# Kernel tuning notes

Measured on AMD Instinct MI355X. Metric: run time of the kernel, lower is better.

## Reference

```python
import jax, jax.numpy as jnp
import numpy as np

B = 4096
SEQ = 128            # window_size * rnn_in_pkts
WINDOW = 32
IN_PKTS = 4
LEN_V, LEN_E = 1500, 64
IPD_V, IPD_E = 256, 64
EV = 64              # embedding_vector_bits
RNN_IN = IN_PKTS * EV   # 256
H = 256              # rnn_hidden_bits
LABELS = 100


def setup_inputs() -> dict:
    key = jax.random.key(0)
    ks = jax.random.split(key, 12)
    s = 0.05
    return {
        "len_x": jax.random.randint(ks[0], (B, SEQ), 0, LEN_V),
        "ipd_x": jax.random.randint(ks[1], (B, SEQ), 0, IPD_V),
        "len_emb": jax.random.normal(ks[2], (LEN_V, LEN_E), jnp.float32) * s,
        "ipd_emb": jax.random.normal(ks[3], (IPD_V, IPD_E), jnp.float32) * s,
        "fc_w": jax.random.normal(ks[4], (EV, LEN_E + IPD_E), jnp.float32) * s,
        "fc_b": jax.random.normal(ks[5], (EV,), jnp.float32) * s,
        "w_ih": jax.random.normal(ks[6], (3 * H, RNN_IN), jnp.float32) * s,
        "w_hh": jax.random.normal(ks[7], (3 * H, H), jnp.float32) * s,
        "b_ih": jax.random.normal(ks[8], (3 * H,), jnp.float32) * s,
        "b_hh": jax.random.normal(ks[9], (3 * H,), jnp.float32) * s,
        "out_w": jax.random.normal(ks[10], (LABELS, H), jnp.float32) * s,
        "out_b": jax.random.normal(ks[11], (LABELS,), jnp.float32) * s,
    }


def _gru_scan(rnn_in, w_ih, w_hh, b_ih, b_hh):
    # rnn_in: [B, T, RNN_IN]. Precompute input-side gates for all steps at once.
    gi_all = jnp.einsum("bti,gi->btg", rnn_in, w_ih) + b_ih  # [B,T,3H]
    h0 = jnp.zeros((rnn_in.shape[0], H), rnn_in.dtype)

    def step(h, gi):
        gh = h @ w_hh.T + b_hh                 # [B,3H]
        i_r, i_z, i_n = jnp.split(gi, 3, axis=-1)
        h_r, h_z, h_n = jnp.split(gh, 3, axis=-1)
        r = jax.nn.sigmoid(i_r + h_r)
        z = jax.nn.sigmoid(i_z + h_z)
        n = jnp.tanh(i_n + r * h_n)
        h_new = (1.0 - z) * n + z * h
        return h_new, None

    h_final, _ = jax.lax.scan(step, h0, jnp.swapaxes(gi_all, 0, 1))
    return h_final


def reference(len_x, ipd_x, len_emb, ipd_emb, fc_w, fc_b, w_ih, w_hh, b_ih, b_hh, out_w, out_b):
    len_e = len_emb[len_x]                      # [B,SEQ,LEN_E]
    ipd_e = ipd_emb[ipd_x]                      # [B,SEQ,IPD_E]
    cat = jnp.concatenate([len_e, ipd_e], axis=-1)
    evs = cat @ fc_w.T + fc_b                   # [B,SEQ,EV]
    rnn_in = evs.reshape(B, WINDOW, RNN_IN)     # [B,32,256]
    h = _gru_scan(rnn_in, w_ih, w_hh, b_ih, b_hh)
    logits = h @ out_w.T + out_b                # [B,LABELS]
    return logits
```

## Files before the change

kernel.cpp:

```cpp
#include <hip/hip_runtime.h>
#include <hip/hip_bf16.h>

typedef __bf16 bf16_t;
typedef __bf16 bf16x8 __attribute__((ext_vector_type(8)));
typedef float f32x4 __attribute__((ext_vector_type(4)));
typedef unsigned short u16x4 __attribute__((ext_vector_type(4)));

#define MFMA16(a, b, c) __builtin_amdgcn_mfma_f32_16x16x32_bf16((a), (b), (c), 0, 0, 0)

#define BATCH 4096
#define SEQN 128
#define HN 256
#define NLABELS 100
#define TSTEPS 32
#define LEN_VN 1500
#define IPD_VN 256

#define OFF_LENT   0u
#define OFF_IPDT   384000u
#define OFF_BRZ    449536u
#define OFF_WIH    451584u
#define OFF_WHH    844800u
#define OFF_GI     1238016u
#define WS_NEEDED  202564608u

__device__ __forceinline__ float sigf(float x) {
    return __builtin_amdgcn_rcpf(1.f + __expf(-x));
}
__device__ __forceinline__ float tanh_fast(float x) {
    return 2.f * __builtin_amdgcn_rcpf(1.f + __expf(-2.f * x)) - 1.f;
}
__device__ __forceinline__ float b2f(unsigned short v) {
    union { unsigned u; float f; } c; c.u = ((unsigned)v) << 16; return c.f;
}
__device__ __forceinline__ unsigned short f2b(float f) {
    union { bf16_t h; unsigned short s; } c; c.h = (bf16_t)f; return c.s;
}

__global__ void prep_kernel(const float* __restrict__ len_emb,
                            const float* __restrict__ ipd_emb,
                            const float* __restrict__ fc_w,
                            const float* __restrict__ fc_b,
                            const float* __restrict__ w_ih,
                            const float* __restrict__ w_hh,
                            const float* __restrict__ b_ih,
                            const float* __restrict__ b_hh,
                            float* __restrict__ lenT, float* __restrict__ ipdT,
                            float* __restrict__ brz,
                            bf16_t* __restrict__ wfrag_ih,
                            bf16_t* __restrict__ wfrag_hh) {
    const int bid = blockIdx.x, tid = threadIdx.x;
    if (bid < 439) {
        const int row = bid * 4 + (tid >> 6);
        const int e = tid & 63;
        if (row < LEN_VN) {
            const float* emb = len_emb + row * 64;
            const float* wv = fc_w + e * 128;
            float s = fc_b[e];
            #pragma unroll 8
            for (int j = 0; j < 64; ++j) s += emb[j] * wv[j];
            lenT[row * 64 + e] = s;
        } else if (row < LEN_VN + IPD_VN) {
            const int v = row - LEN_VN;
            const float* emb = ipd_emb + v * 64;
            const float* wv = fc_w + e * 128 + 64;
            float s = 0.f;
            #pragma unroll 8
            for (int j = 0; j < 64; ++j) s += emb[j] * wv[j];
            ipdT[v * 64 + e] = s;
        }
    } else if (bid < 631) {
        const int flat = (bid - 439) * 256 + tid;
        const int which = flat / 24576;
        const int rem = flat % 24576;
        const int c = rem >> 9;
        const int kt = (rem >> 6) & 7;
        const int lane = rem & 63;
        const int g = c * 16 + (lane & 15);
        const int k0 = kt * 32 + (lane >> 4) * 8;
        const float* src = (which == 0 ? w_ih : w_hh) + g * 256 + k0;
        bf16_t* dst = (which == 0 ? wfrag_ih : wfrag_hh) + ((c * 8 + kt) * 64 + lane) * 8;
        f32x4 s0 = *(const f32x4*)(src);
        f32x4 s1 = *(const f32x4*)(src + 4);
        bf16x8 o;
        #pragma unroll
        for (int j = 0; j < 4; ++j) { o[j] = (bf16_t)s0[j]; o[4 + j] = (bf16_t)s1[j]; }
        *(bf16x8*)dst = o;
    } else {
        const int g = (bid - 631) * 256 + tid;
        if (g < 512) brz[g] = b_ih[g] + b_hh[g];
    }
}

__global__ void __launch_bounds__(512, 2)
gemm_gi(const int* __restrict__ len_x, const int* __restrict__ ipd_x,
        const float* __restrict__ lenT, const float* __restrict__ ipdT,
        const bf16_t* __restrict__ wfrag_ih, bf16_t* __restrict__ gi) {
    __shared__ bf16_t wlds[8 * 8 * 512];
    __shared__ bf16_t a_lds[2][8 * 512];

    const int tid = threadIdx.x;
    const int lane = tid & 63;
    const int w = tid >> 6;
    const int bt = blockIdx.x;

    const int cts[6] = {2*w, 2*w + 1, 16 + 2*w, 17 + 2*w, 32 + 2*w, 33 + 2*w};

    bf16x8 wr[5][8];
    #pragma unroll
    for (int cc = 0; cc < 5; ++cc)
        #pragma unroll
        for (int kt = 0; kt < 8; ++kt)
            wr[cc][kt] = *(const bf16x8*)(wfrag_ih + ((cts[cc] * 8 + kt) * 64 + lane) * 8);
    #pragma unroll
    for (int kt = 0; kt < 8; ++kt)
        *(bf16x8*)&wlds[(w * 8 + kt) * 512 + lane * 8] =
            *(const bf16x8*)(wfrag_ih + ((cts[5] * 8 + kt) * 64 + lane) * 8);

    const int b_row = bt * 16 + (lane & 15);
    const int k0 = w * 32 + (lane >> 4) * 8;
    const int p = k0 >> 6;
    const int e0 = k0 & 63;
    auto do_gather = [&](int t, int buf) {
        const int seq = t * 4 + p;
        const int v1 = len_x[b_row * SEQN + seq];
        const int v2 = ipd_x[b_row * SEQN + seq];
        const f32x4* lp = (const f32x4*)(lenT + v1 * 64 + e0);
        const f32x4* ip = (const f32x4*)(ipdT + v2 * 64 + e0);
        f32x4 a0 = lp[0] + ip[0];
        f32x4 a1 = lp[1] + ip[1];
        bf16x8 o;
        #pragma unroll
        for (int j = 0; j < 4; ++j) { o[j] = (bf16_t)a0[j]; o[4 + j] = (bf16_t)a1[j]; }
        *(bf16x8*)&a_lds[buf][tid * 8] = o;
    };

    do_gather(0, 0);
    bf16_t* gib = gi + (size_t)bt * 32 * 48 * 256 + lane * 4;

    for (int t = 0; t < TSTEPS; ++t) {
        const int cur = t & 1;
        __syncthreads();
        if (t + 1 < TSTEPS) do_gather(t + 1, cur ^ 1);

        f32x4 acc[6] = {};
        #pragma unroll
        for (int kt = 0; kt < 8; ++kt) {
            bf16x8 af = *(const bf16x8*)&a_lds[cur][kt * 512 + lane * 8];
            bf16x8 w5 = *(const bf16x8*)&wlds[(w * 8 + kt) * 512 + lane * 8];
            #pragma unroll
            for (int cc = 0; cc < 5; ++cc)
                acc[cc] = MFMA16(af, wr[cc][kt], acc[cc]);
            acc[5] = MFMA16(af, w5, acc[5]);
        }

        #pragma unroll
        for (int cc = 0; cc < 6; ++cc) {
            u16x4 o;
            #pragma unroll
            for (int r = 0; r < 4; ++r) o[r] = f2b(acc[cc][r]);
            *(u16x4*)(gib + ((size_t)t * 48 + cts[cc]) * 256) = o;
        }
    }
}

__global__ void __launch_bounds__(512, 2)
gru_kernel(const bf16_t* __restrict__ gi,
           const bf16_t* __restrict__ wfrag_hh,
           const float* __restrict__ brz,
           const float* __restrict__ b_ih,
           const float* __restrict__ b_hh,
           const float* __restrict__ out_w,
           const float* __restrict__ out_b,
           float* __restrict__ out) {
    __shared__ bf16_t wlds[8 * 8 * 512];
    __shared__ bf16_t h_lds[8 * 512];
    __shared__ float h_fin[16 * 260];

    const int tid = threadIdx.x;
    const int lane = tid & 63;
    const int w = tid >> 6;
    const int bt = blockIdx.x;
    const int col = lane & 15;
    const int jbase = w * 32;

    const int cts[6] = {2*w, 2*w + 1, 16 + 2*w, 17 + 2*w, 32 + 2*w, 33 + 2*w};

    bf16x8 wr[5][8];
    #pragma unroll
    for (int cc = 0; cc < 5; ++cc)
        #pragma unroll
        for (int kt = 0; kt < 8; ++kt)
            wr[cc][kt] = *(const bf16x8*)(wfrag_hh + ((cts[cc] * 8 + kt) * 64 + lane) * 8);
    #pragma unroll
    for (int kt = 0; kt < 8; ++kt)
        *(bf16x8*)&wlds[(w * 8 + kt) * 512 + lane * 8] =
            *(const bf16x8*)(wfrag_hh + ((cts[5] * 8 + kt) * 64 + lane) * 8);

    for (int i = tid; i < 8 * 512; i += 512) h_lds[i] = (bf16_t)0.f;

    float b_r[2], b_z[2], b_in[2], b_hn[2];
    #pragma unroll
    for (int c2 = 0; c2 < 2; ++c2) {
        const int j = jbase + c2 * 16 + col;
        b_r[c2] = brz[j];
        b_z[c2] = brz[256 + j];
        b_in[c2] = b_ih[512 + j];
        b_hn[c2] = b_hh[512 + j];
    }

    f32x4 hprev[2] = {};
    const bf16_t* gib = gi + (size_t)bt * 32 * 48 * 256 + lane * 4;

    for (int t = 0; t < TSTEPS; ++t) {
        u16x4 g[6];
        #pragma unroll
        for (int cc = 0; cc < 6; ++cc)
            g[cc] = *(const u16x4*)(gib + ((size_t)t * 48 + cts[cc]) * 256);

        f32x4 acc[6] = {};
        __syncthreads();
        #pragma unroll
        for (int kt = 0; kt < 8; ++kt) {
            bf16x8 ah = *(const bf16x8*)&h_lds[kt * 512 + lane * 8];
            bf16x8 w5 = *(const bf16x8*)&wlds[(w * 8 + kt) * 512 + lane * 8];
            #pragma unroll
            for (int cc = 0; cc < 5; ++cc)
                acc[cc] = MFMA16(ah, wr[cc][kt], acc[cc]);
            acc[5] = MFMA16(ah, w5, acc[5]);
        }
        __syncthreads();

        #pragma unroll
        for (int c2 = 0; c2 < 2; ++c2) {
            const int j = jbase + c2 * 16 + col;
            const int kt_j = j >> 5;
            const int lane_j = ((j >> 3) & 3) * 16;
            const int jj = j & 7;
            #pragma unroll
            for (int r = 0; r < 4; ++r) {
                float rg = sigf(acc[c2][r] + b2f(g[c2][r]) + b_r[c2]);
                float zg = sigf(acc[2 + c2][r] + b2f(g[2 + c2][r]) + b_z[c2]);
                float u = b2f(g[4 + c2][r]) + b_in[c2] + rg * (acc[4 + c2][r] + b_hn[c2]);
                float ng = tanh_fast(u);
                float hn = (1.f - zg) * ng + zg * hprev[c2][r];
                hprev[c2][r] = hn;
                const int m = ((lane >> 4) << 2) + r;
                h_lds[kt_j * 512 + (lane_j + m) * 8 + jj] = (bf16_t)hn;
            }
        }
    }

    #pragma unroll
    for (int c2 = 0; c2 < 2; ++c2) {
        const int j = jbase + c2 * 16 + col;
        #pragma unroll
        for (int r = 0; r < 4; ++r) {
            const int m = ((lane >> 4) << 2) + r;
            h_fin[m * 260 + j] = hprev[c2][r];
        }
    }
    __syncthreads();

    for (int i = tid; i < 16 * NLABELS; i += 512) {
        const int row = i / NLABELS;
        const int cl = i - row * NLABELS;
        const f32x4* wrow = (const f32x4*)(out_w + cl * 256);
        const f32x4* hr = (const f32x4*)(h_fin + row * 260);
        f32x4 acc = {0.f, 0.f, 0.f, 0.f};
        #pragma unroll 4
        for (int k = 0; k < 64; ++k) acc += hr[k] * wrow[k];
        out[(bt * 16 + row) * NLABELS + cl] =
            out_b[cl] + acc[0] + acc[1] + acc[2] + acc[3];
    }
}

extern "C" void kernel_launch(void* const* d_in, const int* in_sizes, int n_in,
                              void* d_out, int out_size, void* d_ws, size_t ws_size,
                              hipStream_t stream) {
    (void)in_sizes; (void)n_in; (void)out_size; (void)ws_size;
    const int*   len_x   = (const int*)d_in[0];
    const int*   ipd_x   = (const int*)d_in[1];
    const float* len_emb = (const float*)d_in[2];
    const float* ipd_emb = (const float*)d_in[3];
    const float* fc_w    = (const float*)d_in[4];
    const float* fc_b    = (const float*)d_in[5];
    const float* w_ih    = (const float*)d_in[6];
    const float* w_hh    = (const float*)d_in[7];
    const float* b_ih    = (const float*)d_in[8];
    const float* b_hh    = (const float*)d_in[9];
    const float* out_w   = (const float*)d_in[10];
    const float* out_b   = (const float*)d_in[11];

    char* ws = (char*)d_ws;
    float*  lenT = (float*)(ws + OFF_LENT);
    float*  ipdT = (float*)(ws + OFF_IPDT);
    float*  brz  = (float*)(ws + OFF_BRZ);
    bf16_t* wfi  = (bf16_t*)(ws + OFF_WIH);
    bf16_t* wfh  = (bf16_t*)(ws + OFF_WHH);
    bf16_t* gi   = (bf16_t*)(ws + OFF_GI);

    prep_kernel<<<633, 256, 0, stream>>>(len_emb, ipd_emb, fc_w, fc_b,
                                         w_ih, w_hh, b_ih, b_hh,
                                         lenT, ipdT, brz, wfi, wfh);
    gemm_gi<<<256, 512, 0, stream>>>(len_x, ipd_x, lenT, ipdT, wfi, gi);
    gru_kernel<<<256, 512, 0, stream>>>(gi, wfh, brz, b_ih, b_hh,
                                        out_w, out_b, (float*)d_out);
}
```

Before: 264.9 us.

## Use 16 waves per block for GI GEMM and GRU recurrence, double-buffer hidden state

Both the input-gate GEMM and the GRU kernel now run with 1024 threads (16 waves), so each wave owns one 16-column tile per gate and keeps all its weights in registers, with no LDS weight tile. The GRU step double-buffers h in LDS, which removes one of the two barriers per timestep. Biases are folded into the GI GEMM output and the precombined bias array is dropped from prep. The gi layout changes to gate-tile-major with time inner. The aim is to shorten the serial per-step critical path and raise occupancy, at the cost of more waves contending for barriers.

```diff
diff --git a/kernel.cpp b/kernel.cpp
--- a/kernel.cpp
+++ b/kernel.cpp
@@ -18,11 +18,10 @@
 
 #define OFF_LENT   0u
 #define OFF_IPDT   384000u
-#define OFF_BRZ    449536u
-#define OFF_WIH    451584u
-#define OFF_WHH    844800u
-#define OFF_GI     1238016u
-#define WS_NEEDED  202564608u
+#define OFF_WIH    449536u
+#define OFF_WHH    842752u
+#define OFF_GI     1235968u
+#define WS_NEEDED  202562560u
 
 __device__ __forceinline__ float sigf(float x) {
     return __builtin_amdgcn_rcpf(1.f + __expf(-x));
@@ -43,10 +42,7 @@
                             const float* __restrict__ fc_b,
                             const float* __restrict__ w_ih,
                             const float* __restrict__ w_hh,
-                            const float* __restrict__ b_ih,
-                            const float* __restrict__ b_hh,
                             float* __restrict__ lenT, float* __restrict__ ipdT,
-                            float* __restrict__ brz,
                             bf16_t* __restrict__ wfrag_ih,
                             bf16_t* __restrict__ wfrag_hh) {
     const int bid = blockIdx.x, tid = threadIdx.x;
@@ -69,7 +65,7 @@
             for (int j = 0; j < 64; ++j) s += emb[j] * wv[j];
             ipdT[v * 64 + e] = s;
         }
-    } else if (bid < 631) {
+    } else {
         const int flat = (bid - 439) * 256 + tid;
         const int which = flat / 24576;
         const int rem = flat % 24576;
@@ -86,42 +82,47 @@
         #pragma unroll
         for (int j = 0; j < 4; ++j) { o[j] = (bf16_t)s0[j]; o[4 + j] = (bf16_t)s1[j]; }
         *(bf16x8*)dst = o;
-    } else {
-        const int g = (bid - 631) * 256 + tid;
-        if (g < 512) brz[g] = b_ih[g] + b_hh[g];
-    }
-}
-
-__global__ void __launch_bounds__(512, 2)
+    }
+}
+
+__global__ void __launch_bounds__(1024, 4)
 gemm_gi(const int* __restrict__ len_x, const int* __restrict__ ipd_x,
         const float* __restrict__ lenT, const float* __restrict__ ipdT,
-        const bf16_t* __restrict__ wfrag_ih, bf16_t* __restrict__ gi) {
-    __shared__ bf16_t wlds[8 * 8 * 512];
-    __shared__ bf16_t a_lds[2][8 * 512];
+        const bf16_t* __restrict__ wfrag_ih,
+        const float* __restrict__ b_ih, const float* __restrict__ b_hh,
+        bf16_t* __restrict__ gi) {
+    __shared__ bf16_t a_lds[4][8 * 512];
 
     const int tid = threadIdx.x;
     const int lane = tid & 63;
     const int w = tid >> 6;
     const int bt = blockIdx.x;
-
-    const int cts[6] = {2*w, 2*w + 1, 16 + 2*w, 17 + 2*w, 32 + 2*w, 33 + 2*w};
-
-    bf16x8 wr[5][8];
+    const int col = lane & 15;
+
+    bf16x8 wr[3][8];
     #pragma unroll
-    for (int cc = 0; cc < 5; ++cc)
+    for (int cc = 0; cc < 3; ++cc) {
+        const int ct = cc * 16 + w;
         #pragma unroll
         for (int kt = 0; kt < 8; ++kt)
-            wr[cc][kt] = *(const bf16x8*)(wfrag_ih + ((cts[cc] * 8 + kt) * 64 + lane) * 8);
-    #pragma unroll
-    for (int kt = 0; kt < 8; ++kt)
-        *(bf16x8*)&wlds[(w * 8 + kt) * 512 + lane * 8] =
-            *(const bf16x8*)(wfrag_ih + ((cts[5] * 8 + kt) * 64 + lane) * 8);
-
-    const int b_row = bt * 16 + (lane & 15);
-    const int k0 = w * 32 + (lane >> 4) * 8;
+            wr[cc][kt] = *(const bf16x8*)(wfrag_ih + ((ct * 8 + kt) * 64 + lane) * 8);
+    }
+    float bias[3];
+    bias[0] = b_ih[w * 16 + col] + b_hh[w * 16 + col];
+    bias[1] = b_ih[256 + w * 16 + col] + b_hh[256 + w * 16 + col];
+    bias[2] = b_ih[512 + w * 16 + col];
+
+    const int tt = tid >> 9;
+    const int sub = tid & 511;
+    const int glane = sub & 63;
+    const int gkt = sub >> 6;
+    const int b_row = bt * 16 + (glane & 15);
+    const int k0 = gkt * 32 + (glane >> 4) * 8;
     const int p = k0 >> 6;
     const int e0 = k0 & 63;
-    auto do_gather = [&](int t, int buf) {
+
+    auto do_gather = [&](int pair, int bufbase) {
+        const int t = pair * 2 + tt;
         const int seq = t * 4 + p;
         const int v1 = len_x[b_row * SEQN + seq];
         const int v2 = ipd_x[b_row * SEQN + seq];
@@ -132,49 +133,49 @@
         bf16x8 o;
         #pragma unroll
         for (int j = 0; j < 4; ++j) { o[j] = (bf16_t)a0[j]; o[4 + j] = (bf16_t)a1[j]; }
-        *(bf16x8*)&a_lds[buf][tid * 8] = o;
+        *(bf16x8*)&a_lds[bufbase + tt][sub * 8] = o;
     };
 
     do_gather(0, 0);
-    bf16_t* gib = gi + (size_t)bt * 32 * 48 * 256 + lane * 4;
-
-    for (int t = 0; t < TSTEPS; ++t) {
-        const int cur = t & 1;
+    bf16_t* gib = gi + (size_t)bt * 48 * 32 * 256 + lane * 4;
+
+    for (int pair = 0; pair < 16; ++pair) {
+        const int cur = (pair & 1) * 2;
         __syncthreads();
-        if (t + 1 < TSTEPS) do_gather(t + 1, cur ^ 1);
-
-        f32x4 acc[6] = {};
-        #pragma unroll
-        for (int kt = 0; kt < 8; ++kt) {
-            bf16x8 af = *(const bf16x8*)&a_lds[cur][kt * 512 + lane * 8];
-            bf16x8 w5 = *(const bf16x8*)&wlds[(w * 8 + kt) * 512 + lane * 8];
+        if (pair + 1 < 16) do_gather(pair + 1, 2 - cur);
+
+        #pragma unroll
+        for (int half = 0; half < 2; ++half) {
+            const int t = pair * 2 + half;
+            f32x4 acc[3] = {};
+            const bf16_t* ab = &a_lds[cur + half][lane * 8];
             #pragma unroll
-            for (int cc = 0; cc < 5; ++cc)
-                acc[cc] = MFMA16(af, wr[cc][kt], acc[cc]);
-            acc[5] = MFMA16(af, w5, acc[5]);
-        }
-
-        #pragma unroll
-        for (int cc = 0; cc < 6; ++cc) {
-            u16x4 o;
+            for (int kt = 0; kt < 8; ++kt) {
+                bf16x8 af = *(const bf16x8*)(ab + kt * 512);
+                acc[0] = MFMA16(af, wr[0][kt], acc[0]);
+                acc[1] = MFMA16(af, wr[1][kt], acc[1]);
+                acc[2] = MFMA16(af, wr[2][kt], acc[2]);
+            }
             #pragma unroll
-            for (int r = 0; r < 4; ++r) o[r] = f2b(acc[cc][r]);
-            *(u16x4*)(gib + ((size_t)t * 48 + cts[cc]) * 256) = o;
-        }
-    }
-}
-
-__global__ void __launch_bounds__(512, 2)
+            for (int cc = 0; cc < 3; ++cc) {
+                const int ct = cc * 16 + w;
+                u16x4 o;
+                #pragma unroll
+                for (int r = 0; r < 4; ++r) o[r] = f2b(acc[cc][r] + bias[cc]);
+                *(u16x4*)(gib + ((size_t)ct * 32 + t) * 256) = o;
+            }
+        }
+    }
+}
+
+__global__ void __launch_bounds__(1024, 4)
 gru_kernel(const bf16_t* __restrict__ gi,
            const bf16_t* __restrict__ wfrag_hh,
-           const float* __restrict__ brz,
-           const float* __restrict__ b_ih,
            const float* __restrict__ b_hh,
            const float* __restrict__ out_w,
            const float* __restrict__ out_b,
            float* __restrict__ out) {
-    __shared__ bf16_t wlds[8 * 8 * 512];
-    __shared__ bf16_t h_lds[8 * 512];
+    __shared__ bf16_t h_lds[2][8 * 512];
     __shared__ float h_fin[16 * 260];
 
     const int tid = threadIdx.x;
@@ -182,87 +183,62 @@
     const int w = tid >> 6;
     const int bt = blockIdx.x;
     const int col = lane & 15;
-    const int jbase = w * 32;
-
-    const int cts[6] = {2*w, 2*w + 1, 16 + 2*w, 17 + 2*w, 32 + 2*w, 33 + 2*w};
-
-    bf16x8 wr[5][8];
+
+    bf16x8 wr[3][8];
     #pragma unroll
-    for (int cc = 0; cc < 5; ++cc)
+    for (int cc = 0; cc < 3; ++cc) {
+        const int ct = cc * 16 + w;
         #pragma unroll
         for (int kt = 0; kt < 8; ++kt)
-            wr[cc][kt] = *(const bf16x8*)(wfrag_hh + ((cts[cc] * 8 + kt) * 64 + lane) * 8);
+            wr[cc][kt] = *(const bf16x8*)(wfrag_hh + ((ct * 8 + kt) * 64 + lane) * 8);
+    }
+    const int j = w * 16 + col;
+    const float b_hn = b_hh[512 + j];
+
+    for (int i = tid; i < 8 * 512; i += 1024) h_lds[1][i] = (bf16_t)0.f;
+
+    const int woff = (j >> 5) * 512 + (((j >> 3) & 3) * 16 + (lane >> 4) * 4) * 8 + (j & 7);
+
+    f32x4 hprev = {};
+    const bf16_t* gib = gi + (size_t)bt * 48 * 32 * 256 + lane * 4;
+
+    for (int t = 0; t < TSTEPS; ++t) {
+        u16x4 g0 = *(const u16x4*)(gib + ((size_t)(w) * 32 + t) * 256);
+        u16x4 g1 = *(const u16x4*)(gib + ((size_t)(16 + w) * 32 + t) * 256);
+        u16x4 g2 = *(const u16x4*)(gib + ((size_t)(32 + w) * 32 + t) * 256);
+
+        __syncthreads();
+
+        const bf16_t* hb = &h_lds[(t + 1) & 1][lane * 8];
+        f32x4 acc0 = {}, acc1 = {}, acc2 = {};
+        #pragma unroll
+        for (int kt = 0; kt < 8; ++kt) {
+            bf16x8 ah = *(const bf16x8*)(hb + kt * 512);
+            acc0 = MFMA16(ah, wr[0][kt], acc0);
+            acc1 = MFMA16(ah, wr[1][kt], acc1);
+            acc2 = MFMA16(ah, wr[2][kt], acc2);
+        }
+
+        bf16_t* hw = &h_lds[t & 1][woff];
+        #pragma unroll
+        for (int r = 0; r < 4; ++r) {
+            float rg = sigf(acc0[r] + b2f(g0[r]));
+            float zg = sigf(acc1[r] + b2f(g1[r]));
+            float ng = tanh_fast(b2f(g2[r]) + rg * (acc2[r] + b_hn));
+            float hn = ng + zg * (hprev[r] - ng);
+            hprev[r] = hn;
+            hw[r * 8] = (bf16_t)hn;
+        }
+    }
+
     #pragma unroll
-    for (int kt = 0; kt < 8; ++kt)
-        *(bf16x8*)&wlds[(w * 8 + kt) * 512 + lane * 8] =
-            *(const bf16x8*)(wfrag_hh + ((cts[5] * 8 + kt) * 64 + lane) * 8);
-
-    for (int i = tid; i < 8 * 512; i += 512) h_lds[i] = (bf16_t)0.f;
-
-    float b_r[2], b_z[2], b_in[2], b_hn[2];
-    #pragma unroll
-    for (int c2 = 0; c2 < 2; ++c2) {
-        const int j = jbase + c2 * 16 + col;
-        b_r[c2] = brz[j];
-        b_z[c2] = brz[256 + j];
-        b_in[c2] = b_ih[512 + j];
-        b_hn[c2] = b_hh[512 + j];
-    }
-
-    f32x4 hprev[2] = {};
-    const bf16_t* gib = gi + (size_t)bt * 32 * 48 * 256 + lane * 4;
-
-    for (int t = 0; t < TSTEPS; ++t) {
-        u16x4 g[6];
-        #pragma unroll
-        for (int cc = 0; cc < 6; ++cc)
-            g[cc] = *(const u16x4*)(gib + ((size_t)t * 48 + cts[cc]) * 256);
-
-        f32x4 acc[6] = {};
-        __syncthreads();
-        #pragma unroll
-        for (int kt = 0; kt < 8; ++kt) {
-            bf16x8 ah = *(const bf16x8*)&h_lds[kt * 512 + lane * 8];
-            bf16x8 w5 = *(const bf16x8*)&wlds[(w * 8 + kt) * 512 + lane * 8];
-            #pragma unroll
-            for (int cc = 0; cc < 5; ++cc)
-                acc[cc] = MFMA16(ah, wr[cc][kt], acc[cc]);
-            acc[5] = MFMA16(ah, w5, acc[5]);
-        }
-        __syncthreads();
-
-        #pragma unroll
-        for (int c2 = 0; c2 < 2; ++c2) {
-            const int j = jbase + c2 * 16 + col;
-            const int kt_j = j >> 5;
-            const int lane_j = ((j >> 3) & 3) * 16;
-            const int jj = j & 7;
-            #pragma unroll
-            for (int r = 0; r < 4; ++r) {
-                float rg = sigf(acc[c2][r] + b2f(g[c2][r]) + b_r[c2]);
-                float zg = sigf(acc[2 + c2][r] + b2f(g[2 + c2][r]) + b_z[c2]);
-                float u = b2f(g[4 + c2][r]) + b_in[c2] + rg * (acc[4 + c2][r] + b_hn[c2]);
-                float ng = tanh_fast(u);
-                float hn = (1.f - zg) * ng + zg * hprev[c2][r];
-                hprev[c2][r] = hn;
-                const int m = ((lane >> 4) << 2) + r;
-                h_lds[kt_j * 512 + (lane_j + m) * 8 + jj] = (bf16_t)hn;
-            }
-        }
-    }
-
-    #pragma unroll
-    for (int c2 = 0; c2 < 2; ++c2) {
-        const int j = jbase + c2 * 16 + col;
-        #pragma unroll
-        for (int r = 0; r < 4; ++r) {
-            const int m = ((lane >> 4) << 2) + r;
-            h_fin[m * 260 + j] = hprev[c2][r];
-        }
+    for (int r = 0; r < 4; ++r) {
+        const int m = (lane >> 4) * 4 + r;
+        h_fin[m * 260 + j] = hprev[r];
     }
     __syncthreads();
 
-    for (int i = tid; i < 16 * NLABELS; i += 512) {
+    for (int i = tid; i < 16 * NLABELS; i += 1024) {
         const int row = i / NLABELS;
         const int cl = i - row * NLABELS;
         const f32x4* wrow = (const f32x4*)(out_w + cl * 256);
@@ -295,15 +271,14 @@
     char* ws = (char*)d_ws;
     float*  lenT = (float*)(ws + OFF_LENT);
     float*  ipdT = (float*)(ws + OFF_IPDT);
-    float*  brz  = (float*)(ws + OFF_BRZ);
     bf16_t* wfi  = (bf16_t*)(ws + OFF_WIH);
     bf16_t* wfh  = (bf16_t*)(ws + OFF_WHH);
     bf16_t* gi   = (bf16_t*)(ws + OFF_GI);
 
-    prep_kernel<<<633, 256, 0, stream>>>(len_emb, ipd_emb, fc_w, fc_b,
-                                         w_ih, w_hh, b_ih, b_hh,
-                                         lenT, ipdT, brz, wfi, wfh);
-    gemm_gi<<<256, 512, 0, stream>>>(len_x, ipd_x, lenT, ipdT, wfi, gi);
-    gru_kernel<<<256, 512, 0, stream>>>(gi, wfh, brz, b_ih, b_hh,
-                                        out_w, out_b, (float*)d_out);
-}
+    prep_kernel<<<631, 256, 0, stream>>>(len_emb, ipd_emb, fc_w, fc_b,
+                                         w_ih, w_hh, lenT, ipdT, wfi, wfh);
+    gemm_gi<<<256, 1024, 0, stream>>>(len_x, ipd_x, lenT, ipdT, wfi,
+                                      b_ih, b_hh, gi);
+    gru_kernel<<<256, 1024, 0, stream>>>(gi, wfh, b_hh, out_w, out_b,
+                                         (float*)d_out);
+}
```

Measured after the change: 383.5 us. +44.8%, slower.
